# Optimization experiments

Measured on AMD Instinct MI355X. Metric: run time of the kernel, lower is better.

Reference implementation:

```python
import jax, jax.numpy as jnp
import numpy as np

KSIZE = 3
STRIDE = 1
PADDING = 1
DILATION = 1
C_IN = 16
C_OUT = 16


def setup_inputs() -> dict:
    key = jax.random.key(0)
    k1, k2, k3 = jax.random.split(key, 3)
    inputs = jax.random.normal(k1, (2, C_IN, 24, 24, 24, 24), dtype=jnp.float32)
    weight = jax.random.normal(k2, (C_OUT, C_IN * KSIZE ** 4), dtype=jnp.float32)
    bias = jax.random.normal(k3, (1, C_OUT, 1, 1, 1, 1), dtype=jnp.float32)
    return {"inputs": inputs, "weight": weight, "bias": bias}


def reference(inputs, weight, bias):
    # weight stored flattened: [C_out, C_in * k^4] -> [C_out, C_in, k, k, k, k]
    w = weight.reshape(C_OUT, C_IN, KSIZE, KSIZE, KSIZE, KSIZE)
    # General 4-spatial-dim convolution via XLA's ND conv.
    dn = jax.lax.ConvDimensionNumbers(
        lhs_spec=(0, 1, 2, 3, 4, 5),   # N, C, U, V, H, W
        rhs_spec=(0, 1, 2, 3, 4, 5),   # O, I, kU, kV, kH, kW
        out_spec=(0, 1, 2, 3, 4, 5),
    )
    out = jax.lax.conv_general_dilated(
        inputs, w,
        window_strides=(STRIDE,) * 4,
        padding=((PADDING, PADDING),) * 4,
        rhs_dilation=(DILATION,) * 4,
        dimension_numbers=dn,
    )
    return out + bias
```

## Files before the change

### kernel.cpp

```cpp
#include <hip/hip_runtime.h>

#define S 24
#define PLANE 576
#define CISTRIDE 331776
#define SLAB_B 21632
#define QSLAB_B 4992
#define QOFF 3328
#define A_BYTES 46080
#define WS_SLABS A_BYTES

typedef __attribute__((ext_vector_type(8))) short bf16x8;
typedef __attribute__((ext_vector_type(4))) float f32x4;

__device__ __forceinline__ ushort f2bf(float f) {
    unsigned int u = __builtin_bit_cast(unsigned int, f);
    unsigned int r = u + 0x7fffu + ((u >> 16) & 1u);
    return (ushort)(r >> 16);
}

__global__ void __launch_bounds__(256)
pack_in(const float* __restrict__ in, const float* __restrict__ wgt, char* __restrict__ ws) {
    __shared__ __align__(16) float lds_f[16 * 576];

    const int b = blockIdx.x;
    const int nb = b / PLANE, uv = b % PLANE;
    const float* src = in + (size_t)nb * 16 * CISTRIDE + (size_t)uv * PLANE;
    char* dst = ws + WS_SLABS + (size_t)b * SLAB_B;
    const int t = threadIdx.x;

    #pragma unroll
    for (int r = 0; r < 9; ++r) {
        int chunk = r * 256 + t;
        int ci = chunk / 144, q4 = chunk % 144;
        __builtin_amdgcn_global_load_lds(
            (const __attribute__((address_space(1))) unsigned int*)(src + (size_t)ci * CISTRIDE + 4 * q4),
            (__attribute__((address_space(3))) unsigned int*)(&lds_f[chunk * 4]),
            16, 0, 0);
    }
    __syncthreads();

    #pragma unroll
    for (int i = 0; i < 6; ++i) {
        int c = i * 256 + t;
        if (c < 1352) {
            int pos = c >> 1, h = c & 1;
            int row = pos / 26, col = pos % 26;
            uint4 o = make_uint4(0, 0, 0, 0);
            if (row >= 1 && row <= 24 && col >= 1 && col <= 24) {
                int q = (row - 1) * 24 + (col - 1);
                #pragma unroll
                for (int kk = 0; kk < 4; ++kk) {
                    float fa = lds_f[(8 * h + 2 * kk) * 576 + q];
                    float fb = lds_f[(8 * h + 2 * kk + 1) * 576 + q];
                    ((unsigned*)&o)[kk] = (unsigned)f2bf(fa) | ((unsigned)f2bf(fb) << 16);
                }
            }
            *(uint4*)(dst + (((size_t)c * 16) ^ (size_t)((row & 3) << 4))) = o;
        }
    }

    if (b == 0) {
        for (int i = t; i < 2880; i += 256) {
            int step = i >> 6;
            int tap = step / 5, s = step % 5;
            int lane = i & 63;
            int co = lane & 15, gA = lane >> 4;
            int o = 2 * s + (gA >> 1);
            int cib = (gA & 1) * 8;
            ushort vals[8];
            #pragma unroll
            for (int j = 0; j < 8; ++j)
                vals[j] = (o <= 8) ? f2bf(wgt[co * 1296 + (cib + j) * 81 + tap * 9 + o]) : (ushort)0;
            uint4 pk;
            pk.x = vals[0] | ((unsigned)vals[1] << 16);
            pk.y = vals[2] | ((unsigned)vals[3] << 16);
            pk.z = vals[4] | ((unsigned)vals[5] << 16);
            pk.w = vals[6] | ((unsigned)vals[7] << 16);
            *(uint4*)(ws + (size_t)i * 16) = pk;
        }
    }
}

__global__ void __launch_bounds__(192, 4)
conv4d_main(const char* __restrict__ ws, const float* __restrict__ bias,
            float* __restrict__ out) {
    __shared__ __align__(16) char lds[2 * QSLAB_B];

    const int t = threadIdx.x, lane = t & 63, wvid = t >> 6;
    const int braw = blockIdx.x;
    const int b = (braw & 7) * 216 + (braw >> 3);
    const int nb = b / 864, rem = b % 864;
    const int u = rem / 36, rem2 = rem % 36;
    const int v0 = (rem2 / 6) * 4, qq = rem2 % 6;

    const int n16 = lane & 15, g = lane >> 4;
    const int dh = n16 >> 3, dw = n16 & 7;
    const int half = g & 1, osel = g >> 1;

    int loff[2][5];
    #pragma unroll
    for (int tr = 0; tr < 2; ++tr)
        #pragma unroll
        for (int s = 0; s < 5; ++s) {
            int o = 2 * s + osel; if (o > 8) o = 8;
            int kh = o / 3, kw = o % 3;
            int r_off = dh + kh, c_off = dw + kw;
            int lin = (r_off * 26 + c_off) * 32 + half * 16;
            loff[tr][s] = lin ^ (((tr * 2 + r_off) & 3) << 4);
        }

    f32x4 acc[4][2];
    #pragma unroll
    for (int a = 0; a < 4; ++a)
        #pragma unroll
        for (int tr = 0; tr < 2; ++tr) acc[a][tr] = (f32x4){0, 0, 0, 0};

    unsigned mask = 0;
    #pragma unroll
    for (int i = 0; i < 18; ++i) {
        int uu = u + i / 6 - 1, vv = v0 + i % 6 - 1;
        if (uu >= 0 && uu < S && vv >= 0 && vv < S) mask |= 1u << i;
    }

    const char* slabs = ws + WS_SLABS;
    const size_t qoff = (size_t)qq * QOFF;
    #define SLAB_PTR(i_) (slabs + ((size_t)nb * PLANE + (u + (i_) / 6 - 1) * S + (v0 + (i_) % 6 - 1)) * SLAB_B + qoff)

    #define STAGE(bufsel_, src_) do {                                              \
        const char* _s = (src_);                                                   \
        _Pragma("unroll")                                                          \
        for (int r2 = 0; r2 < 2; ++r2) {                                           \
            int chunk = r2 * 192 + t;                                              \
            if (r2 < 1 || t < 120)                                                 \
                __builtin_amdgcn_global_load_lds(                                  \
                    (const __attribute__((address_space(1))) unsigned int*)(_s + (size_t)chunk * 16), \
                    (__attribute__((address_space(3))) unsigned int*)(lds + (bufsel_) * QSLAB_B + chunk * 16), \
                    16, 0, 0);                                                     \
        }                                                                          \
    } while (0)

    int first = __ffs(mask) - 1;
    STAGE(0, SLAB_PTR(first));
    __syncthreads();

    int cb = 0;
    bf16x8 afr[3][5];

    #pragma unroll
    for (int ku = 0; ku < 3; ++ku) {
        if (!((mask >> (ku * 6)) & 63u)) continue;
        #pragma unroll
        for (int kv = 0; kv < 3; ++kv) {
            const char* ap = ws + (size_t)(ku * 3 + kv) * 5120 + (size_t)lane * 16;
            #pragma unroll
            for (int s = 0; s < 5; ++s) afr[kv][s] = *(const bf16x8*)(ap + s * 1024);
        }
        #pragma unroll
        for (int vj = 0; vj < 6; ++vj) {
            const int i = ku * 6 + vj;
            if (!(mask & (1u << i))) continue;
            unsigned rm = mask >> (i + 1);
            int nx = rm ? (i + 1 + __ffs(rm) - 1) : -1;
            if (nx >= 0) STAGE(cb ^ 1, SLAB_PTR(nx));

            const char* bp = lds + cb * QSLAB_B + wvid * 256;
            #pragma unroll
            for (int tr = 0; tr < 2; ++tr) {
                #pragma unroll
                for (int s = 0; s < 5; ++s) {
                    bf16x8 bfr = *(const bf16x8*)(bp + tr * 1664 + loff[tr][s]);
                    #pragma unroll
                    for (int kv = 0; kv < 3; ++kv) {
                        const int a = vj - kv;
                        if (a >= 0 && a <= 3)
                            acc[a][tr] = __builtin_amdgcn_mfma_f32_16x16x32_bf16(afr[kv][s], bfr, acc[a][tr], 0, 0, 0);
                    }
                }
            }
            __syncthreads();
            cb ^= 1;
        }
    }

    float bv[4];
    #pragma unroll
    for (int r = 0; r < 4; ++r) bv[r] = bias[g * 4 + r];
    #pragma unroll
    for (int a = 0; a < 4; ++a) {
        float* outp = out + (size_t)nb * 16 * CISTRIDE + (size_t)(u * S + v0 + a) * PLANE;
        #pragma unroll
        for (int tr = 0; tr < 2; ++tr) {
            int row = qq * 4 + tr * 2 + dh;
            int col = wvid * 8 + dw;
            int pos = row * S + col;
            #pragma unroll
            for (int r = 0; r < 4; ++r)
                outp[(size_t)(g * 4 + r) * CISTRIDE + pos] = acc[a][tr][r] + bv[r];
        }
    }
}

extern "C" void kernel_launch(void* const* d_in, const int* in_sizes, int n_in,
                              void* d_out, int out_size, void* d_ws, size_t ws_size,
                              hipStream_t stream) {
    const float* in   = (const float*)d_in[0];
    const float* wgt  = (const float*)d_in[1];
    const float* bias = (const float*)d_in[2];
    float* out        = (float*)d_out;
    char* ws          = (char*)d_ws;

    pack_in<<<dim3(1152), dim3(256), 0, stream>>>(in, wgt, ws);
    conv4d_main<<<dim3(1728), dim3(192), 0, stream>>>(ws, bias, out);
}
```

Baseline: 71.62 us.

## Deepen slab staging to two-ahead prefetch with explicit vmcnt waits

The fully unrolled ku/vj loop becomes a runtime while-loop over the set bits of the neighbour mask. Each slab is now staged two iterations ahead, using explicit s_waitcnt vmcnt and raw barriers instead of __syncthreads, so global-to-LDS copies can overlap with more MFMA work. The trade-off is that vj and ku become runtime values, so accumulator indexing and the MFMA guards may no longer resolve at compile time, which risks register spills or selection chains. The fixed vmcnt(2) count also assumes two loads per stage, but threads with t>=120 issue only one, so the wait may not guarantee the current slab has fully arrived.

```diff
diff --git a/kernel.cpp b/kernel.cpp
--- a/kernel.cpp
+++ b/kernel.cpp
@@ -139,47 +139,53 @@
         }                                                                          \
     } while (0)
 
-    int first = __ffs(mask) - 1;
-    STAGE(0, SLAB_PTR(first));
-    __syncthreads();
+    int w0 = __ffs(mask) - 1;
+    unsigned m1 = mask & (mask - 1);
+    STAGE(0, SLAB_PTR(w0));
+    if (m1) { int w1 = __ffs(m1) - 1; STAGE(1, SLAB_PTR(w1)); }
 
     int cb = 0;
+    int prev_row = -1;
     bf16x8 afr[3][5];
-
-    #pragma unroll
-    for (int ku = 0; ku < 3; ++ku) {
-        if (!((mask >> (ku * 6)) & 63u)) continue;
-        #pragma unroll
-        for (int kv = 0; kv < 3; ++kv) {
-            const char* ap = ws + (size_t)(ku * 3 + kv) * 5120 + (size_t)lane * 16;
-            #pragma unroll
-            for (int s = 0; s < 5; ++s) afr[kv][s] = *(const bf16x8*)(ap + s * 1024);
-        }
-        #pragma unroll
-        for (int vj = 0; vj < 6; ++vj) {
-            const int i = ku * 6 + vj;
-            if (!(mask & (1u << i))) continue;
-            unsigned rm = mask >> (i + 1);
-            int nx = rm ? (i + 1 + __ffs(rm) - 1) : -1;
-            if (nx >= 0) STAGE(cb ^ 1, SLAB_PTR(nx));
-
-            const char* bp = lds + cb * QSLAB_B + wvid * 256;
-            #pragma unroll
-            for (int tr = 0; tr < 2; ++tr) {
+    unsigned mrem = mask;
+
+    while (mrem) {
+        const int i = __ffs(mrem) - 1; mrem &= mrem - 1;
+        const unsigned mn2 = mrem ? (mrem & (mrem - 1)) : 0;
+        const int n2 = mn2 ? (__ffs(mn2) - 1) : -1;
+
+        if (mrem) asm volatile("s_waitcnt vmcnt(2)" ::: "memory");
+        else      asm volatile("s_waitcnt vmcnt(0)" ::: "memory");
+        __builtin_amdgcn_s_barrier();
+
+        const int ku = i / 6, vj = i % 6;
+        if (ku != prev_row) {
+            prev_row = ku;
+            #pragma unroll
+            for (int kv = 0; kv < 3; ++kv) {
+                const char* ap = ws + (size_t)(ku * 3 + kv) * 5120 + (size_t)lane * 16;
                 #pragma unroll
-                for (int s = 0; s < 5; ++s) {
-                    bf16x8 bfr = *(const bf16x8*)(bp + tr * 1664 + loff[tr][s]);
-                    #pragma unroll
-                    for (int kv = 0; kv < 3; ++kv) {
-                        const int a = vj - kv;
-                        if (a >= 0 && a <= 3)
-                            acc[a][tr] = __builtin_amdgcn_mfma_f32_16x16x32_bf16(afr[kv][s], bfr, acc[a][tr], 0, 0, 0);
-                    }
+                for (int s = 0; s < 5; ++s) afr[kv][s] = *(const bf16x8*)(ap + s * 1024);
+            }
+        }
+
+        const char* bp = lds + cb * QSLAB_B + wvid * 256;
+        #pragma unroll
+        for (int tr = 0; tr < 2; ++tr) {
+            #pragma unroll
+            for (int s = 0; s < 5; ++s) {
+                bf16x8 bfr = *(const bf16x8*)(bp + tr * 1664 + loff[tr][s]);
+                #pragma unroll
+                for (int kv = 0; kv < 3; ++kv) {
+                    const int a = vj - kv;
+                    if (a >= 0 && a <= 3)
+                        acc[a][tr] = __builtin_amdgcn_mfma_f32_16x16x32_bf16(afr[kv][s], bfr, acc[a][tr], 0, 0, 0);
                 }
             }
-            __syncthreads();
-            cb ^= 1;
-        }
+        }
+        __builtin_amdgcn_s_barrier();
+        if (n2 >= 0) STAGE(cb, SLAB_PTR(n2));
+        cb ^= 1;
     }
 
     float bv[4];
```

New measurement: 105.0 us. +46.6%, slower.

## Deepen slab prefetch to two windows with fixed loop and manual vmcnt waits

Applied to the files above, without the earlier changes.

Replaces the mask-driven double-buffered slab loop with a fixed 18-window loop that keeps two slab stages in flight. Pointers are clamped so every window issues its loads, and explicit s_waitcnt vmcnt plus raw s_barrier replace __syncthreads. The goal is to hide global-to-LDS latency behind MFMA work and to remove the data-dependent control flow. In exchange, edge blocks load slabs they never use, and each staged buffer is enlarged and may read past the quarter-slab region.

```diff
diff --git a/kernel.cpp b/kernel.cpp
--- a/kernel.cpp
+++ b/kernel.cpp
@@ -4,7 +4,7 @@
 #define PLANE 576
 #define CISTRIDE 331776
 #define SLAB_B 21632
-#define QSLAB_B 4992
+#define QBUF_B 6144
 #define QOFF 3328
 #define A_BYTES 46080
 #define WS_SLABS A_BYTES
@@ -84,7 +84,7 @@
 __global__ void __launch_bounds__(192, 4)
 conv4d_main(const char* __restrict__ ws, const float* __restrict__ bias,
             float* __restrict__ out) {
-    __shared__ __align__(16) char lds[2 * QSLAB_B];
+    __shared__ __align__(16) char lds[2 * QBUF_B];
 
     const int t = threadIdx.x, lane = t & 63, wvid = t >> 6;
     const int braw = blockIdx.x;
@@ -124,46 +124,46 @@
 
     const char* slabs = ws + WS_SLABS;
     const size_t qoff = (size_t)qq * QOFF;
-    #define SLAB_PTR(i_) (slabs + ((size_t)nb * PLANE + (u + (i_) / 6 - 1) * S + (v0 + (i_) % 6 - 1)) * SLAB_B + qoff)
-
-    #define STAGE(bufsel_, src_) do {                                              \
-        const char* _s = (src_);                                                   \
-        _Pragma("unroll")                                                          \
-        for (int r2 = 0; r2 < 2; ++r2) {                                           \
-            int chunk = r2 * 192 + t;                                              \
-            if (r2 < 1 || t < 120)                                                 \
-                __builtin_amdgcn_global_load_lds(                                  \
-                    (const __attribute__((address_space(1))) unsigned int*)(_s + (size_t)chunk * 16), \
-                    (__attribute__((address_space(3))) unsigned int*)(lds + (bufsel_) * QSLAB_B + chunk * 16), \
-                    16, 0, 0);                                                     \
-        }                                                                          \
+    #define SPTR(w_) (slabs + ((size_t)nb * PLANE                                        \
+        + (size_t)min(max(u + (w_) / 6 - 1, 0), 23) * S                                  \
+        + (size_t)min(max(v0 + (w_) % 6 - 1, 0), 23)) * SLAB_B + qoff)
+
+    #define STAGE(bufsel_, src_) do {                                                    \
+        const char* _s = (src_);                                                         \
+        _Pragma("unroll")                                                                \
+        for (int r2 = 0; r2 < 2; ++r2) {                                                 \
+            int chunk = r2 * 192 + t;                                                    \
+            __builtin_amdgcn_global_load_lds(                                            \
+                (const __attribute__((address_space(1))) unsigned int*)(_s + (size_t)chunk * 16), \
+                (__attribute__((address_space(3))) unsigned int*)(lds + (bufsel_) * QBUF_B + chunk * 16), \
+                16, 0, 0);                                                               \
+        }                                                                                \
     } while (0)
 
-    int first = __ffs(mask) - 1;
-    STAGE(0, SLAB_PTR(first));
-    __syncthreads();
-
-    int cb = 0;
+    STAGE(0, SPTR(0));
+    STAGE(1, SPTR(1));
+
     bf16x8 afr[3][5];
 
     #pragma unroll
-    for (int ku = 0; ku < 3; ++ku) {
-        if (!((mask >> (ku * 6)) & 63u)) continue;
-        #pragma unroll
-        for (int kv = 0; kv < 3; ++kv) {
-            const char* ap = ws + (size_t)(ku * 3 + kv) * 5120 + (size_t)lane * 16;
-            #pragma unroll
-            for (int s = 0; s < 5; ++s) afr[kv][s] = *(const bf16x8*)(ap + s * 1024);
-        }
-        #pragma unroll
-        for (int vj = 0; vj < 6; ++vj) {
-            const int i = ku * 6 + vj;
-            if (!(mask & (1u << i))) continue;
-            unsigned rm = mask >> (i + 1);
-            int nx = rm ? (i + 1 + __ffs(rm) - 1) : -1;
-            if (nx >= 0) STAGE(cb ^ 1, SLAB_PTR(nx));
-
-            const char* bp = lds + cb * QSLAB_B + wvid * 256;
+    for (int w = 0; w < 18; ++w) {
+        if (w <= 16) asm volatile("s_waitcnt vmcnt(2)" ::: "memory");
+        else         asm volatile("s_waitcnt vmcnt(0)" ::: "memory");
+        __builtin_amdgcn_s_barrier();
+
+        if ((w % 6) == 0) {
+            const int ku = w / 6;
+            #pragma unroll
+            for (int kv = 0; kv < 3; ++kv) {
+                const char* ap = ws + (size_t)(ku * 3 + kv) * 5120 + (size_t)lane * 16;
+                #pragma unroll
+                for (int s = 0; s < 5; ++s) afr[kv][s] = *(const bf16x8*)(ap + s * 1024);
+            }
+        }
+
+        if (mask & (1u << w)) {
+            const int vj = w % 6;
+            const char* bp = lds + (w & 1) * QBUF_B + wvid * 256;
             #pragma unroll
             for (int tr = 0; tr < 2; ++tr) {
                 #pragma unroll
@@ -177,9 +177,9 @@
                     }
                 }
             }
-            __syncthreads();
-            cb ^= 1;
-        }
+        }
+        __builtin_amdgcn_s_barrier();
+        if (w + 2 < 18) STAGE(w & 1, SPTR(w + 2));
     }
 
     float bv[4];
```

New measurement: 68.83 us. 3.9% less time.
